# Optimization experiments

Hardware: AMD Instinct MI355X
Metric: run time of the kernel (lower is better)

The kernel has to match this reference:

```python
import jax, jax.numpy as jnp
import numpy as np

B, N_ELEC, N_NUC, F = 4096, 64, 16, 128
CUTOFF = 5.0  # hardcoded in original forward (radius(e, n, 5.0))


def setup_inputs() -> dict:
    key = jax.random.key(0)
    k1, k2, k3, k4 = jax.random.split(key, 4)
    return {
        "s_nuc": jax.random.normal(k1, (B, N_NUC, F), jnp.float32),
        "v_nuc": jax.random.normal(k2, (B, N_NUC, 3, F), jnp.float32),
        "coord_elec": jax.random.normal(k3, (B, N_ELEC, 3), jnp.float32) * 3.0,
        "coord_nuc": jax.random.normal(k4, (N_NUC, 3), jnp.float32) * 3.0,
    }


def reference(s_nuc, v_nuc, coord_elec, coord_nuc):
    # Per-sample bipartite radius graph nuc->elec, then PyG-style batching
    # (node indices offset by n_nuc / n_elec per graph). Since jit requires
    # static shapes, we emit the dense set of all (nuc, elec) pairs plus a
    # boolean mask marking edges within the cutoff radius.
    b_dim, n_elec = coord_elec.shape[:2]
    n_nuc = coord_nuc.shape[0]
    f = s_nuc.shape[-1]

    # diff[b, i, j, :] = coord_elec[b, j] - coord_nuc[i]  (== elec[col] - nuc[row])
    diff = coord_elec[:, None, :, :] - coord_nuc[None, :, None, :]  # [B, n_nuc, n_elec, 3]
    dist = jnp.linalg.norm(diff, axis=-1)                            # [B, n_nuc, n_elec]
    mask = (dist < CUTOFF).reshape(-1)                               # [B*n_nuc*n_elec]

    bidx = jnp.arange(b_dim)[:, None, None]
    row = bidx * n_nuc + jnp.arange(n_nuc)[None, :, None]   # nuc index (batched)
    col = bidx * n_elec + jnp.arange(n_elec)[None, None, :]  # elec index (batched)
    row = jnp.broadcast_to(row, (b_dim, n_nuc, n_elec)).reshape(-1)
    col = jnp.broadcast_to(col, (b_dim, n_nuc, n_elec)).reshape(-1)
    edge_index = jnp.stack([row, col])                        # [2, B*n_nuc*n_elec]

    edge_attr = diff.reshape(-1, 3)
    s_flat = s_nuc.reshape(b_dim * n_nuc, f)
    v_flat = v_nuc.reshape(b_dim * n_nuc, 3, f)
    return (s_flat, v_flat, edge_index, edge_attr, mask)
```

## Files before the change

kernel.cpp:

```cpp
#include <hip/hip_runtime.h>
#include <math.h>

#define BB 4096
#define N_ELEC 64
#define N_NUC 16
#define FF 128
#define CUTOFF 5.0f

typedef float v4f __attribute__((ext_vector_type(4)));

static constexpr long long S_SIZE = (long long)BB * N_NUC * FF;
static constexpr long long V_SIZE = (long long)BB * N_NUC * 3 * FF;
static constexpr long long E_CNT  = (long long)BB * N_NUC * N_ELEC;

static constexpr long long OFF_EI = S_SIZE + V_SIZE;
static constexpr long long OFF_EA = OFF_EI + 2 * E_CNT;
static constexpr long long OFF_M  = OFF_EA + 3 * E_CNT;

static constexpr int COPY_BLOCKS = (int)((S_SIZE + V_SIZE) / 4 / 256);
static constexpr int EDGE_BLOCKS = (int)(E_CNT / 256);

__global__ __launch_bounds__(256) void fused_kernel(
    const v4f* __restrict__ s, const v4f* __restrict__ v,
    const float* __restrict__ coord_elec,
    const float* __restrict__ coord_nuc,
    float* __restrict__ out)
{
    const int bid = blockIdx.x;
    const int t = threadIdx.x;

    if (bid < COPY_BLOCKS) {
        long long i = (long long)bid * 256 + t;
        constexpr long long S4 = S_SIZE / 4;
        v4f val = (i < S4) ? __builtin_nontemporal_load(&s[i])
                           : __builtin_nontemporal_load(&v[i - S4]);
        __builtin_nontemporal_store(val, &((v4f*)out)[i]);
        return;
    }

    __shared__ float nuc[N_NUC * 3];
    __shared__ float elec[N_ELEC * 3];
    __shared__ float attr[256 * 3];

    const long long e0 = (long long)(bid - COPY_BLOCKS) * 256;
    const int b = (int)(e0 >> 10);

    if (t < 48) nuc[t] = coord_nuc[t];
    if (t >= 64 && t < 64 + 192)
        elec[t - 64] = coord_elec[(long long)b * (N_ELEC * 3) + (t - 64)];
    __syncthreads();

    const long long e = e0 + t;
    const int i = (int)((e >> 6) & 15);
    const int j = t & 63;

    float d0 = elec[j * 3 + 0] - nuc[i * 3 + 0];
    float d1 = elec[j * 3 + 1] - nuc[i * 3 + 1];
    float d2 = elec[j * 3 + 2] - nuc[i * 3 + 2];

    attr[t * 3 + 0] = d0;
    attr[t * 3 + 1] = d1;
    attr[t * 3 + 2] = d2;

    __builtin_nontemporal_store((float)(b * N_NUC + i),  &out[OFF_EI + e]);
    __builtin_nontemporal_store((float)(b * N_ELEC + j), &out[OFF_EI + E_CNT + e]);
    float dist = sqrtf(d0 * d0 + d1 * d1 + d2 * d2);
    __builtin_nontemporal_store(dist < CUTOFF ? 1.0f : 0.0f, &out[OFF_M + e]);

    __syncthreads();

    if (t < 192) {
        v4f* dst = (v4f*)(out + OFF_EA + e0 * 3);
        __builtin_nontemporal_store(((const v4f*)attr)[t], &dst[t]);
    }
}

extern "C" void kernel_launch(void* const* d_in, const int* in_sizes, int n_in,
                              void* d_out, int out_size, void* d_ws, size_t ws_size,
                              hipStream_t stream) {
    const float* s_nuc      = (const float*)d_in[0];
    const float* v_nuc      = (const float*)d_in[1];
    const float* coord_elec = (const float*)d_in[2];
    const float* coord_nuc  = (const float*)d_in[3];
    float* out = (float*)d_out;

    fused_kernel<<<COPY_BLOCKS + EDGE_BLOCKS, 256, 0, stream>>>(
        (const v4f*)s_nuc, (const v4f*)v_nuc, coord_elec, coord_nuc, out);
}
```

Baseline: 319.2 us.

## Vectorize edge stores per thread, widen copy blocks, and reorder block roles

Each edge block now covers one whole batch sample (1024 edges), and each thread computes 4 consecutive edges. The thread writes row, column and mask as 16-byte vector stores and packs edge_attr directly into three float4 stores, which removes the shared-memory staging and the second barrier. Copy blocks now move 4 float4s per thread with plain loads, which cuts the block count, and edge blocks are scheduled first. The trade-off is more registers per thread and fewer blocks overall.

```diff
diff --git a/kernel.cpp b/kernel.cpp
--- a/kernel.cpp
+++ b/kernel.cpp
@@ -17,8 +17,12 @@
 static constexpr long long OFF_EA = OFF_EI + 2 * E_CNT;
 static constexpr long long OFF_M  = OFF_EA + 3 * E_CNT;
 
-static constexpr int COPY_BLOCKS = (int)((S_SIZE + V_SIZE) / 4 / 256);
-static constexpr int EDGE_BLOCKS = (int)(E_CNT / 256);
+static constexpr long long S4 = S_SIZE / 4;
+static constexpr long long V4 = V_SIZE / 4;
+
+static constexpr int EDGE_BLOCKS = BB;
+static constexpr int COPY_BLOCKS = (int)((S4 + V4) / 1024);
+static constexpr int S_COPY_BLOCKS = (int)(S4 / 1024);
 
 __global__ __launch_bounds__(256) void fused_kernel(
     const v4f* __restrict__ s, const v4f* __restrict__ v,
@@ -29,50 +33,67 @@
     const int bid = blockIdx.x;
     const int t = threadIdx.x;
 
-    if (bid < COPY_BLOCKS) {
-        long long i = (long long)bid * 256 + t;
-        constexpr long long S4 = S_SIZE / 4;
-        v4f val = (i < S4) ? __builtin_nontemporal_load(&s[i])
-                           : __builtin_nontemporal_load(&v[i - S4]);
-        __builtin_nontemporal_store(val, &((v4f*)out)[i]);
+    if (bid >= EDGE_BLOCKS) {
+        const int cb = bid - EDGE_BLOCKS;
+        const long long g = (long long)cb * 1024 + t;
+        const v4f* __restrict__ src = (cb < S_COPY_BLOCKS) ? (s + g) : (v + (g - S4));
+        v4f a0 = src[0];
+        v4f a1 = src[256];
+        v4f a2 = src[512];
+        v4f a3 = src[768];
+        v4f* dst = (v4f*)out + g;
+        __builtin_nontemporal_store(a0, dst);
+        __builtin_nontemporal_store(a1, dst + 256);
+        __builtin_nontemporal_store(a2, dst + 512);
+        __builtin_nontemporal_store(a3, dst + 768);
         return;
     }
 
     __shared__ float nuc[N_NUC * 3];
     __shared__ float elec[N_ELEC * 3];
-    __shared__ float attr[256 * 3];
 
-    const long long e0 = (long long)(bid - COPY_BLOCKS) * 256;
-    const int b = (int)(e0 >> 10);
-
+    const int b = bid;
     if (t < 48) nuc[t] = coord_nuc[t];
     if (t >= 64 && t < 64 + 192)
         elec[t - 64] = coord_elec[(long long)b * (N_ELEC * 3) + (t - 64)];
     __syncthreads();
 
-    const long long e = e0 + t;
-    const int i = (int)((e >> 6) & 15);
-    const int j = t & 63;
+    const int i  = t >> 4;
+    const int j0 = (t & 15) << 2;
+    const long long e = (long long)b * 1024 + ((long long)t << 2);
 
-    float d0 = elec[j * 3 + 0] - nuc[i * 3 + 0];
-    float d1 = elec[j * 3 + 1] - nuc[i * 3 + 1];
-    float d2 = elec[j * 3 + 2] - nuc[i * 3 + 2];
+    const float nx = nuc[i * 3 + 0];
+    const float ny = nuc[i * 3 + 1];
+    const float nz = nuc[i * 3 + 2];
 
-    attr[t * 3 + 0] = d0;
-    attr[t * 3 + 1] = d1;
-    attr[t * 3 + 2] = d2;
+    float d[4][3];
+    v4f msk;
+    #pragma unroll
+    for (int k = 0; k < 4; ++k) {
+        const float dx = elec[(j0 + k) * 3 + 0] - nx;
+        const float dy = elec[(j0 + k) * 3 + 1] - ny;
+        const float dz = elec[(j0 + k) * 3 + 2] - nz;
+        d[k][0] = dx; d[k][1] = dy; d[k][2] = dz;
+        const float dist = sqrtf(dx * dx + dy * dy + dz * dz);
+        msk[k] = dist < CUTOFF ? 1.0f : 0.0f;
+    }
 
-    __builtin_nontemporal_store((float)(b * N_NUC + i),  &out[OFF_EI + e]);
-    __builtin_nontemporal_store((float)(b * N_ELEC + j), &out[OFF_EI + E_CNT + e]);
-    float dist = sqrtf(d0 * d0 + d1 * d1 + d2 * d2);
-    __builtin_nontemporal_store(dist < CUTOFF ? 1.0f : 0.0f, &out[OFF_M + e]);
+    const float rowf = (float)(b * N_NUC + i);
+    const v4f row = {rowf, rowf, rowf, rowf};
+    const float c0 = (float)(b * N_ELEC + j0);
+    const v4f col = {c0, c0 + 1.0f, c0 + 2.0f, c0 + 3.0f};
 
-    __syncthreads();
+    __builtin_nontemporal_store(row, (v4f*)(out + OFF_EI + e));
+    __builtin_nontemporal_store(col, (v4f*)(out + OFF_EI + E_CNT + e));
+    __builtin_nontemporal_store(msk, (v4f*)(out + OFF_M + e));
 
-    if (t < 192) {
-        v4f* dst = (v4f*)(out + OFF_EA + e0 * 3);
-        __builtin_nontemporal_store(((const v4f*)attr)[t], &dst[t]);
-    }
+    const v4f a0 = {d[0][0], d[0][1], d[0][2], d[1][0]};
+    const v4f a1 = {d[1][1], d[1][2], d[2][0], d[2][1]};
+    const v4f a2 = {d[2][2], d[3][0], d[3][1], d[3][2]};
+    v4f* ap = (v4f*)(out + OFF_EA + e * 3);
+    __builtin_nontemporal_store(a0, ap + 0);
+    __builtin_nontemporal_store(a1, ap + 1);
+    __builtin_nontemporal_store(a2, ap + 2);
 }
 
 extern "C" void kernel_launch(void* const* d_in, const int* in_sizes, int n_in,
@@ -84,6 +105,6 @@
     const float* coord_nuc  = (const float*)d_in[3];
     float* out = (float*)d_out;
 
-    fused_kernel<<<COPY_BLOCKS + EDGE_BLOCKS, 256, 0, stream>>>(
+    fused_kernel<<<EDGE_BLOCKS + COPY_BLOCKS, 256, 0, stream>>>(
         (const v4f*)s_nuc, (const v4f*)v_nuc, coord_elec, coord_nuc, out);
 }
```

Result: slower. 348.5 us (+9.2%).
